# Optimization experiments

Measured on AMD Instinct MI355X. Metric: run time of the kernel, lower is better.

The kernel has to match this reference:

```python
import jax, jax.numpy as jnp
import numpy as np
from jax import lax

B, DIM, HEADS, H, W = 8, 384, 8, 64, 64
HEAD_C = DIM // HEADS        # 48 -> topk k's: 24, 32, 36, 38
HID = int(DIM * 2.66)        # 1021
EPS_LN = 1e-5
EPS_N = 1e-12
SMALL = 1e-6


def conv2d(x, w, b, pad, groups=1):
    out = lax.conv_general_dilated(
        x, w, (1, 1), [(pad, pad), (pad, pad)],
        feature_group_count=groups,
        dimension_numbers=('NCHW', 'OIHW', 'NCHW'))
    return out + b[None, :, None, None]


def l2n(x):
    # torch F.normalize(dim=-1): x / max(||x||_2, eps)
    n = jnp.linalg.norm(x, axis=-1, keepdims=True)
    return x / jnp.maximum(n, EPS_N)


def layer_norm_c(x, w, b):
    # WithBias LayerNorm over channel dim (module does to_3d -> LN(c) -> to_4d)
    xt = jnp.transpose(x, (0, 2, 3, 1))  # b h w c
    mu = xt.mean(-1, keepdims=True)
    var = xt.var(-1, keepdims=True)      # unbiased=False
    y = (xt - mu) / jnp.sqrt(var + EPS_LN) * w + b
    return jnp.transpose(y, (0, 3, 1, 2))


def setup_inputs() -> dict:
    key = jax.random.key(0)
    ks = iter(jax.random.split(key, 40))
    rn = lambda shape, s=0.02: jax.random.normal(next(ks), shape, jnp.float32) * s
    return dict(
        x=jax.random.normal(next(ks), (B, DIM, H, W), jnp.float32),
        spf=jax.random.normal(next(ks), (1, 3, H, W), jnp.float32),
        ln1_w=jnp.ones((DIM,)), ln1_b=jnp.zeros((DIM,)),
        qkv_w=rn((3 * DIM, DIM, 1, 1)), qkv_b=jnp.zeros((3 * DIM,)),
        qkvdw_w=rn((3 * DIM, 1, 3, 3)), qkvdw_b=jnp.zeros((3 * DIM,)),
        proj_w=rn((DIM, 3, 3, 3)), proj_b=jnp.zeros((DIM,)),
        temperature=jnp.ones((HEADS, 1, 1)),
        a1=jnp.array([0.2]), a2=jnp.array([0.2]),
        a3=jnp.array([0.2]), a4=jnp.array([0.2]),
        wmix=jnp.ones((2,)),
        pout_w=rn((DIM, DIM, 1, 1)), pout_b=jnp.zeros((DIM,)),
        ln2_w=jnp.ones((DIM,)), ln2_b=jnp.zeros((DIM,)),
        pin_w=rn((2 * HID, DIM, 1, 1)), pin_b=jnp.zeros((2 * HID,)),
        dw_w=rn((HID, 1, 3, 3)), dw_b=jnp.zeros((HID,)),
        lin_w=rn((HID, HID)), lin_b=jnp.zeros((HID,)),
        adj_w=rn((HID, 2 * HID, 1, 1)), adj_b=jnp.zeros((HID,)),
        fout_w=rn((DIM, HID, 1, 1)), fout_b=jnp.zeros((DIM,)),
    )


def reference(x, spf, ln1_w, ln1_b, qkv_w, qkv_b, qkvdw_w, qkvdw_b,
              proj_w, proj_b, temperature, a1, a2, a3, a4, wmix,
              pout_w, pout_b, ln2_w, ln2_b, pin_w, pin_b, dw_w, dw_b,
              lin_w, lin_b, adj_w, adj_b, fout_w, fout_b):
    # ---------- Attention ----------
    xn = layer_norm_c(x, ln1_w, ln1_b)
    qkv = conv2d(conv2d(xn, qkv_w, qkv_b, 0), qkvdw_w, qkvdw_b, 1, groups=3 * DIM)
    q, k, v = jnp.split(qkv, 3, axis=1)
    q1 = l2n(q)                               # normalize along W axis
    spm = conv2d(jnp.broadcast_to(l2n(spf), (B, 3, H, W)), proj_w, proj_b, 1)
    qs = l2n((q1 * spm).reshape(B, HEADS, HEAD_C, H * W))
    kr = l2n(k.reshape(B, HEADS, HEAD_C, H * W))
    vr = v.reshape(B, HEADS, HEAD_C, H * W)
    attn = jnp.einsum('bhcn,bhdn->bhcd', qs, kr) * temperature[None]

    def masked_sm(kk):
        thr = lax.top_k(attn, kk)[0][..., -1:]  # k-th largest per row
        return jax.nn.softmax(jnp.where(attn >= thr, attn, attn * SMALL), axis=-1)

    attn0 = jax.nn.relu(attn)
    wsm = jax.nn.softmax(wmix)
    topks = [HEAD_C // 2, 2 * HEAD_C // 3, 3 * HEAD_C // 4, 4 * HEAD_C // 5]
    out = jnp.zeros((B, HEADS, HEAD_C, H * W), attn.dtype)
    for kk, c in zip(topks, [a1, a2, a3, a4]):
        blend = attn0 * wsm[0] + masked_sm(kk) * wsm[1]
        out = out + c * jnp.einsum('bhcd,bhdn->bhcn', blend, vr)
    out = out.reshape(B, DIM, H, W)
    x = x + conv2d(out, pout_w, pout_b, 0)

    # ---------- FeedForward ----------
    xn2 = layer_norm_c(x, ln2_w, ln2_b)
    p = conv2d(xn2, pin_w, pin_b, 0)
    x1, x2 = jnp.split(p, 2, axis=1)
    x1d = conv2d(x1, dw_w, dw_b, 1, groups=HID)
    x2l = jnp.einsum('bchw,oc->bohw', x2, lin_w) + lin_b[None, :, None, None]
    cat = jnp.concatenate([x1d, x2l], axis=1)    # [B, 2*HID, H, W]
    y1 = conv2d(cat, adj_w, adj_b, 0)
    y2 = y1  # second cat is identical under the intended (non-buggy) reading
    f = jax.nn.gelu(y1, approximate=False) * y2
    return x + conv2d(f, fout_w, fout_b, 0)
```

## Files before the change

### kernel.cpp

```cpp
#include <hip/hip_runtime.h>
#include <math.h>

typedef long long i64;
typedef unsigned short u16;
typedef unsigned int u32;

#define DIMC 384
#define DIM3 1152
#define HC 48
#define HWN 4096

using bf16x8 = __attribute__((ext_vector_type(8))) short;
using f32x4 = __attribute__((ext_vector_type(4))) float;

__device__ __forceinline__ float bf2f(u16 u) { u32 x = ((u32)u) << 16; return __uint_as_float(x); }
__device__ __forceinline__ u16 f2bf(float f) {
  u32 u = __float_as_uint(f);
  u32 r = u + 0x7FFFu + ((u >> 16) & 1u);
  return (u16)(r >> 16);
}

__device__ __forceinline__ void gld_lds16(const u16* g, u16* l) {
  __builtin_amdgcn_global_load_lds(
      (const __attribute__((address_space(1))) void*)g,
      (__attribute__((address_space(3))) void*)l, 16, 0, 0);
}


__global__ void zero_kernel(float* __restrict__ p, int n) {
  int i = blockIdx.x * 256 + threadIdx.x;
  if (i < n) p[i] = 0.f;
}

__device__ __forceinline__ float ld_as_f(const float* p) { return *p; }
__device__ __forceinline__ float ld_as_f(const u16* p) { return bf2f(*p); }

template <typename T>
__global__ void stats_kernel(const T* __restrict__ x, float* __restrict__ mu,
                             float* __restrict__ rs, int npix4) {
  int idx = blockIdx.x * 256 + threadIdx.x;
  if (idx >= npix4) return;
  int pg = idx * 4;
  int b = pg >> 12, p = pg & 4095;
  const T* xp = x + ((i64)b * DIMC) * HWN + p;
  float s0 = 0.f, s1 = 0.f, s2 = 0.f, s3 = 0.f;
  float q0 = 0.f, q1 = 0.f, q2 = 0.f, q3 = 0.f;
  for (int c = 0; c < DIMC; ++c) {
    const T* rp = xp + (i64)c * HWN;
    float v0 = ld_as_f(rp), v1 = ld_as_f(rp + 1), v2 = ld_as_f(rp + 2), v3 = ld_as_f(rp + 3);
    s0 += v0; s1 += v1; s2 += v2; s3 += v3;
    q0 += v0 * v0; q1 += v1 * v1; q2 += v2 * v2; q3 += v3 * v3;
  }
  const float inv = 1.f / DIMC;
  float4 m = make_float4(s0 * inv, s1 * inv, s2 * inv, s3 * inv);
  float4 r;
  r.x = rsqrtf(q0 * inv - m.x * m.x + 1e-5f);
  r.y = rsqrtf(q1 * inv - m.y * m.y + 1e-5f);
  r.z = rsqrtf(q2 * inv - m.z * m.z + 1e-5f);
  r.w = rsqrtf(q3 * inv - m.w * m.w + 1e-5f);
  *(float4*)(mu + (i64)pg) = m;
  *(float4*)(rs + (i64)pg) = r;
}

template <typename T>
__global__ __launch_bounds__(256) void ln_t_kernel(
    const T* __restrict__ x, const float* __restrict__ mu, const float* __restrict__ rs,
    const float* __restrict__ g, const float* __restrict__ bb, u16* __restrict__ y) {
  __shared__ u16 tile[64][66];
  int p0 = blockIdx.x * 64, c0 = blockIdx.y * 64, b = blockIdx.z;
  int t = threadIdx.x;
  int tp = t & 63, tq = t >> 6;
  float m = mu[b * 4096 + p0 + tp], r = rs[b * 4096 + p0 + tp];
  const T* xp = x + (i64)b * DIMC * HWN + (i64)c0 * 4096 + p0;
#pragma unroll
  for (int i = 0; i < 16; ++i) {
    int c = tq + i * 4;
    float v = ld_as_f(xp + (i64)c * 4096 + tp);
    tile[c][tp] = f2bf((v - m) * r * g[c0 + c] + bb[c0 + c]);
  }
  __syncthreads();
#pragma unroll
  for (int i = 0; i < 16; ++i) {
    int p = tq + i * 4;
    y[((i64)b * 4096 + p0 + p) * 384 + c0 + tp] = tile[tp][p];
  }
}

__global__ __launch_bounds__(256) void dw8_kernel(const u16* __restrict__ in, int ldin,
                                                  const float* __restrict__ w,
                                                  const float* __restrict__ bias,
                                                  u16* __restrict__ out, int ldo, int CH) {
  int t = threadIdx.x;
  int g = t & 31;
  int s = t >> 5;
  int c0 = (blockIdx.y * 32 + g) * 4;
  if (c0 >= ldo) return;
  i64 p0 = (i64)blockIdx.x * 32 + s * 4;
  i64 pb = p0 & ~4095LL;
  int sp = (int)(p0 & 4095);
  int y = sp >> 6, x0 = sp & 63;
  float wv[9][4];
  float acc[4][4];
#pragma unroll
  for (int cc = 0; cc < 4; ++cc) {
    bool val = (c0 + cc) < CH;
    float bv = val ? bias[c0 + cc] : 0.f;
#pragma unroll
    for (int i = 0; i < 4; ++i) acc[i][cc] = bv;
#pragma unroll
    for (int j = 0; j < 9; ++j) wv[j][cc] = val ? w[(c0 + cc) * 9 + j] : 0.f;
  }
#pragma unroll
  for (int dy = 0; dy < 3; ++dy) {
    int yy = y - 1 + dy;
    if ((unsigned)yy >= 64u) continue;
    float row[6][4];
#pragma unroll
    for (int dx = 0; dx < 6; ++dx) {
      int xx = x0 - 1 + dx;
      if ((unsigned)xx < 64u) {
        ushort4 v = *(const ushort4*)(in + (pb + yy * 64 + xx) * ldin + c0);
        row[dx][0] = bf2f(v.x); row[dx][1] = bf2f(v.y);
        row[dx][2] = bf2f(v.z); row[dx][3] = bf2f(v.w);
      } else {
        row[dx][0] = 0.f; row[dx][1] = 0.f; row[dx][2] = 0.f; row[dx][3] = 0.f;
      }
    }
#pragma unroll
    for (int i = 0; i < 4; ++i)
#pragma unroll
      for (int dx = 0; dx < 3; ++dx)
#pragma unroll
        for (int cc = 0; cc < 4; ++cc)
          acc[i][cc] += row[i + dx][cc] * wv[dy * 3 + dx][cc];
  }
#pragma unroll
  for (int i = 0; i < 4; ++i) {
    ushort4 o;
    o.x = (c0 + 0 < CH) ? f2bf(acc[i][0]) : (u16)0;
    o.y = (c0 + 1 < CH) ? f2bf(acc[i][1]) : (u16)0;
    o.z = (c0 + 2 < CH) ? f2bf(acc[i][2]) : (u16)0;
    o.w = (c0 + 3 < CH) ? f2bf(acc[i][3]) : (u16)0;
    *(ushort4*)(out + (p0 + i) * ldo + c0) = o;
  }
}

__global__ __launch_bounds__(192) void dwqnorm_kernel(
    const u16* __restrict__ qkv, const float* __restrict__ w9,
    const float* __restrict__ bias, const float* __restrict__ spm,
    const u16* __restrict__ kv, u16* __restrict__ QS,
    float* __restrict__ qssq, float* __restrict__ kssq) {
  int y = blockIdx.x;
  int b = blockIdx.y;
  int c = blockIdx.z * 192 + threadIdx.x;
  float wv[9];
#pragma unroll
  for (int j = 0; j < 9; ++j) wv[j] = w9[c * 9 + j];
  float bv = bias[c];
  float acc[64];
#pragma unroll
  for (int i = 0; i < 64; ++i) acc[i] = bv;
  i64 rowbase = (i64)b * 4096;
#pragma unroll
  for (int dy = 0; dy < 3; ++dy) {
    int yy = y - 1 + dy;
    if ((unsigned)yy >= 64u) continue;
    const u16* rp = qkv + (rowbase + yy * 64) * 1152 + c;
    float w0 = wv[dy * 3 + 0], w1 = wv[dy * 3 + 1], w2 = wv[dy * 3 + 2];
#pragma unroll
    for (int xi = 0; xi < 64; ++xi) {
      float v = bf2f(rp[(i64)xi * 1152]);
      if (xi > 0) acc[xi - 1] += v * w2;
      acc[xi] += v * w1;
      if (xi < 63) acc[xi + 1] += v * w0;
    }
  }
  float qs = 0.f;
#pragma unroll
  for (int i = 0; i < 64; ++i) qs += acc[i] * acc[i];
  float rw = 1.f / fmaxf(sqrtf(qs), 1e-12f);
  float ps = 0.f;
  const float* sp = spm + (i64)(y * 64) * 384 + c;
  u16* qp = QS + (rowbase + y * 64) * 384 + c;
#pragma unroll
  for (int i = 0; i < 64; ++i) {
    float u = acc[i] * rw * sp[(i64)i * 384];
    qp[(i64)i * 384] = f2bf(u);
    ps += u * u;
  }
  atomicAdd(&qssq[b * 384 + c], ps);
  float ks = 0.f;
  const u16* kp = kv + (rowbase + y * 64) * 768 + c;
#pragma unroll
  for (int i = 0; i < 64; ++i) {
    float kvv = bf2f(kp[(i64)i * 768]);
    ks += kvv * kvv;
  }
  atomicAdd(&kssq[b * 384 + c], ks);
}

__global__ void l2row_kernel(const float* __restrict__ in, float* __restrict__ out) {
  int r = blockIdx.x;
  int lane = threadIdx.x;
  float v = in[r * 64 + lane];
  float ss = v * v;
  for (int o = 32; o > 0; o >>= 1) ss += __shfl_xor(ss, o);
  float n = fmaxf(sqrtf(ss), 1e-12f);
  out[r * 64 + lane] = v / n;
}

__global__ void spm_kernel(const float* __restrict__ s, const float* __restrict__ w,
                           const float* __restrict__ bias, float* __restrict__ out) {
  int idx = blockIdx.x * 256 + threadIdx.x;
  int c = idx % 384, p = idx / 384;
  int xc = p & 63, yr = p >> 6;
  const float* wp = w + c * 27;
  float acc = bias[c];
  for (int ic = 0; ic < 3; ++ic)
    for (int dy = -1; dy <= 1; ++dy) {
      int yy = yr + dy; if ((unsigned)yy >= 64u) continue;
      for (int dx = -1; dx <= 1; ++dx) {
        int xx = xc + dx; if ((unsigned)xx >= 64u) continue;
        acc += s[ic * 4096 + yy * 64 + xx] * wp[ic * 9 + (dy + 1) * 3 + (dx + 1)];
      }
    }
  out[idx] = acc;
}

__global__ __launch_bounds__(256) void attnS_kernel(const u16* __restrict__ QS,
                                                    const u16* __restrict__ kv,
                                                    float* __restrict__ attnP) {
  int ksp = blockIdx.x;
  int bh = blockIdx.y;
  int b = bh >> 3, h = bh & 7;
  __shared__ float qsm[64][49];
  __shared__ float ksm[64][49];
  int t = threadIdx.x, tc = t & 15, td = t >> 4;
  float acc[3][3] = {{0.f}};
  for (int sub = 0; sub < 4; ++sub) {
    i64 nb = (i64)b * 4096 + ksp * 256 + sub * 64;
    __syncthreads();
    for (int l = t; l < 4096; l += 256) {
      int row = l >> 6, cq = l & 63;
      if (cq < 48) {
        qsm[row][cq] = bf2f(QS[(nb + row) * 384 + h * 48 + cq]);
        ksm[row][cq] = bf2f(kv[(nb + row) * 768 + h * 48 + cq]);
      }
    }
    __syncthreads();
#pragma unroll 4
    for (int nn = 0; nn < 64; ++nn) {
      float a0 = qsm[nn][tc], a1 = qsm[nn][tc + 16], a2 = qsm[nn][tc + 32];
      float b0 = ksm[nn][td], b1 = ksm[nn][td + 16], b2 = ksm[nn][td + 32];
      acc[0][0] += a0 * b0; acc[0][1] += a0 * b1; acc[0][2] += a0 * b2;
      acc[1][0] += a1 * b0; acc[1][1] += a1 * b1; acc[1][2] += a1 * b2;
      acc[2][0] += a2 * b0; acc[2][1] += a2 * b1; acc[2][2] += a2 * b2;
    }
  }
  float* ap = attnP + ((i64)bh * 16 + ksp) * 2304;
#pragma unroll
  for (int i = 0; i < 3; ++i)
#pragma unroll
    for (int j = 0; j < 3; ++j)
      ap[(tc + 16 * i) * HC + (td + 16 * j)] = acc[i][j];
}

__global__ void blend_kernel(const float* __restrict__ attnP, const float* __restrict__ qssq,
                             const float* __restrict__ kssq, const float* __restrict__ temp,
                             const float* __restrict__ wmix, const float* __restrict__ pa1,
                             const float* __restrict__ pa2, const float* __restrict__ pa3,
                             const float* __restrict__ pa4, float* __restrict__ comb) {
  int row = blockIdx.x * 4 + (threadIdx.x >> 6);
  int lane = threadIdx.x & 63;
  int bh = row / 48, cc = row - bh * 48;
  int b = bh >> 3, h = bh & 7;
  float a;
  if (lane < 48) {
    const float* pp = attnP + ((i64)bh * 16) * 2304 + cc * 48 + lane;
    float s = 0.f;
#pragma unroll
    for (int sp = 0; sp < 16; ++sp) s += pp[(i64)sp * 2304];
    float qn = 1.f / fmaxf(sqrtf(qssq[b * 384 + h * 48 + cc]), 1e-12f);
    float kn = 1.f / fmaxf(sqrtf(kssq[b * 384 + h * 48 + lane]), 1e-12f);
    a = s * qn * kn * temp[h];
  } else {
    a = -INFINITY;
  }
  int rank = 0;
  for (int j = 0; j < 48; ++j) {
    float aj = __shfl(a, j);
    rank += (aj > a) ? 1 : 0;
  }
  float w0 = wmix[0], w1 = wmix[1];
  float wm = fmaxf(w0, w1);
  float e0 = expf(w0 - wm), e1 = expf(w1 - wm);
  float ws0 = e0 / (e0 + e1), ws1 = e1 / (e0 + e1);
  float c1 = pa1[0], c2 = pa2[0], c3 = pa3[0], c4 = pa4[0];
  float outv = ws0 * (c1 + c2 + c3 + c4) * fmaxf(a, 0.f);
  const int kks[4] = {24, 32, 36, 38};
  const float cs[4] = {c1, c2, c3, c4};
#pragma unroll
  for (int q = 0; q < 4; ++q) {
    float mv = (lane < 48) ? ((rank < kks[q]) ? a : a * 1e-6f) : -INFINITY;
    float mx = mv;
    for (int o = 32; o > 0; o >>= 1) mx = fmaxf(mx, __shfl_xor(mx, o));
    float e = (lane < 48) ? expf(mv - mx) : 0.f;
    float s = e;
    for (int o = 32; o > 0; o >>= 1) s += __shfl_xor(s, o);
    outv += ws1 * cs[q] * (e / s);
  }
  if (lane < 48) comb[(i64)row * 48 + lane] = outv;
}

__global__ __launch_bounds__(384) void combv_kernel(const u16* __restrict__ kv,
                                                    const float* __restrict__ comb,
                                                    u16* __restrict__ AO) {
  __shared__ float Vs[4][8][49];
  i64 p0 = (i64)blockIdx.x * 4;
  int b = (int)(p0 >> 12);
  int t = threadIdx.x;
  int h = t / 48, cc = t - h * 48;
#pragma unroll
  for (int px = 0; px < 4; ++px)
    Vs[px][h][cc] = bf2f(kv[(p0 + px) * 768 + 384 + t]);
  __syncthreads();
  float cr[48];
  const float* cp = comb + ((i64)(b * 8 + h) * 48 + cc) * 48;
#pragma unroll
  for (int d = 0; d < 48; d += 4) {
    float4 v = *(const float4*)(cp + d);
    cr[d] = v.x; cr[d + 1] = v.y; cr[d + 2] = v.z; cr[d + 3] = v.w;
  }
#pragma unroll
  for (int px = 0; px < 4; ++px) {
    float s = 0.f;
#pragma unroll
    for (int d = 0; d < 48; ++d) s += cr[d] * Vs[px][h][d];
    AO[(p0 + px) * 384 + t] = f2bf(s);
  }
}

__global__ void matvec_kernel(const float* __restrict__ Wm, int ldw, int koff,
                              const float* __restrict__ v, const float* __restrict__ add,
                              float* __restrict__ out, int K) {
  int ro = blockIdx.x;
  int t = threadIdx.x;
  const float* wp = Wm + (i64)ro * ldw + koff;
  float s = 0.f;
  for (int k = t; k < K; k += 256) s += wp[k] * v[k];
  __shared__ float sred[256];
  sred[t] = s;
  __syncthreads();
  for (int o = 128; o > 0; o >>= 1) {
    if (t < o) sred[t] += sred[t + o];
    __syncthreads();
  }
  if (t == 0) out[ro] = sred[0] + (add ? add[ro] : 0.f);
}

__global__ __launch_bounds__(256) void gemm64_kernel(
    const float* __restrict__ W, int ldw,
    const float* __restrict__ X,
    float* __restrict__ Y,
    int M, int N, int K, int ksplit) {
  int nt = blockIdx.x, mt = blockIdx.y;
  int ks = blockIdx.z;
  int kchunk = (((K + ksplit - 1) / ksplit) + 15) & ~15;
  int kbeg = ks * kchunk;
  int kend = min(K, kbeg + kchunk);
  __shared__ float As[16][68];
  __shared__ float Bs[16][68];
  int t = threadIdx.x, tx = t & 15, ty = t >> 4;
  int m0 = mt * 64, n0 = nt * 64;
  float acc[4][4];
#pragma unroll
  for (int i = 0; i < 4; ++i)
#pragma unroll
    for (int j = 0; j < 4; ++j) acc[i][j] = 0.f;
  for (int k0 = kbeg; k0 < kend; k0 += 16) {
    int kk = t & 15;
#pragma unroll
    for (int r = 0; r < 4; ++r) {
      int mm = (t >> 4) + r * 16;
      int gm = m0 + mm, gk = k0 + kk;
      As[kk][mm] = (gm < M && gk < kend) ? W[(i64)gm * ldw + gk] : 0.f;
    }
    int nn = t & 63;
#pragma unroll
    for (int r = 0; r < 4; ++r) {
      int k2 = (t >> 6) + r * 4;
      int gk = k0 + k2;
      Bs[k2][nn] = (gk < kend && n0 + nn < N) ? X[(i64)gk * N + n0 + nn] : 0.f;
    }
    __syncthreads();
#pragma unroll
    for (int kk3 = 0; kk3 < 16; ++kk3) {
      float4 av = *(const float4*)&As[kk3][ty * 4];
      float4 bv = *(const float4*)&Bs[kk3][tx * 4];
      float aa[4] = {av.x, av.y, av.z, av.w};
      float bb2[4] = {bv.x, bv.y, bv.z, bv.w};
#pragma unroll
      for (int i = 0; i < 4; ++i)
#pragma unroll
        for (int j = 0; j < 4; ++j) acc[i][j] += aa[i] * bb2[j];
    }
    __syncthreads();
  }
#pragma unroll
  for (int i = 0; i < 4; ++i) {
    int gm = m0 + ty * 4 + i;
    if (gm >= M || n0 + tx * 4 >= N) continue;
    for (int j = 0; j < 4; ++j) atomicAdd(&Y[(i64)gm * N + n0 + tx * 4 + j], acc[i][j]);
  }
}

__global__ void pack_w_kernel(const float* __restrict__ W, int ldw, int koff, int M, int K,
                              int KS, u16* __restrict__ out, int nfrag) {
  int tid = blockIdx.x * 256 + threadIdx.x;
  int lane = tid & 63;
  int idx = tid >> 6;
  if (idx >= nfrag * KS) return;
  int ks = idx % KS, fm = idx / KS;
  int row = fm * 16 + (lane & 15);
  int kb = ks * 32 + (lane >> 4) * 8;
  union { u16 us[8]; uint4 q; } u;
#pragma unroll
  for (int j = 0; j < 8; ++j) {
    int k = kb + j;
    u.us[j] = (row < M && k < K) ? f2bf(W[(i64)row * ldw + koff + k]) : (u16)0;
  }
  *(uint4*)(out + (i64)idx * 512 + lane * 8) = u.q;
}

template <int NF>
__global__ __launch_bounds__(NF * 32) void gemm_nk_kernel(
    const u16* __restrict__ A1, int lda1, int KS1, const u16* __restrict__ Wp1,
    const u16* __restrict__ A2, int lda2, int KS2, const u16* __restrict__ Wp2,
    int nfrag, const float* __restrict__ bias,
    const void* __restrict__ Res, float* __restrict__ Yf, u16* __restrict__ Yh,
    int ldo, int M, int epi) {
  __shared__ __align__(16) u16 Ls[2][NF + 8][512];
  int t = threadIdx.x, lane = t & 63, w = t >> 6;
  int wn = w >> 1, wm = w & 1;
  i64 n0 = (i64)blockIdx.x * (NF * 16);
  int mt = blockIdx.y;

  f32x4 acc[4][4];
#pragma unroll
  for (int i = 0; i < 4; ++i)
#pragma unroll
    for (int r = 0; r < 4; ++r) acc[i][r] = (f32x4){0.f, 0.f, 0.f, 0.f};

  auto stage = [&](int kt, int buf) {
    const u16* A; int lda; const u16* Wp; int KSc; int ks;
    if (kt < KS1) { A = A1; lda = lda1; Wp = Wp1; KSc = KS1; ks = kt; }
    else { A = A2; lda = lda2; Wp = Wp2; KSc = KS2; ks = kt - KS1; }
#pragma unroll
    for (int j = 0; j < 2; ++j) {
      int f = w * 2 + j;
      const u16* srcA = A + (n0 + f * 16 + (lane & 15)) * (i64)lda + ks * 32 + (lane >> 4) * 8;
      gld_lds16(srcA, &Ls[buf][f][0]);
    }
    if constexpr (NF == 8) {
#pragma unroll
      for (int j = 0; j < 2; ++j) {
        int f = w * 2 + j;
        int fmc = min(mt * 8 + f, nfrag - 1);
        gld_lds16(Wp + ((i64)fmc * KSc + ks) * 512 + lane * 8, &Ls[buf][NF + f][0]);
      }
    } else {
      int fmc = min(mt * 8 + w, nfrag - 1);
      gld_lds16(Wp + ((i64)fmc * KSc + ks) * 512 + lane * 8, &Ls[buf][NF + w][0]);
    }
  };

  int KT = KS1 + KS2;
  stage(0, 0);
  __syncthreads();
  int s = 0;
  for (int kt = 0; kt < KT; ++kt) {
    if (kt + 1 < KT) stage(kt + 1, s ^ 1);
    bf16x8 af[4], wf[4];
#pragma unroll
    for (int i = 0; i < 4; ++i) {
      af[i] = *reinterpret_cast<const bf16x8*>(&Ls[s][wn * 4 + i][lane * 8]);
      wf[i] = *reinterpret_cast<const bf16x8*>(&Ls[s][NF + wm * 4 + i][lane * 8]);
    }
#pragma unroll
    for (int i = 0; i < 4; ++i)
#pragma unroll
      for (int r = 0; r < 4; ++r)
        acc[i][r] = __builtin_amdgcn_mfma_f32_16x16x32_bf16(af[i], wf[r], acc[i][r], 0, 0, 0);
    __syncthreads();
    s ^= 1;
  }

#pragma unroll
  for (int i = 0; i < 4; ++i) {
    int nbase = (int)n0 + (wn * 4 + i) * 16 + ((lane >> 4) << 2);
#pragma unroll
    for (int r = 0; r < 4; ++r) {
      int m = mt * 128 + (wm * 4 + r) * 16 + (lane & 15);
      if (epi == 1 || epi == 3) {
        if (m < M) {
          float bv = bias[m];
          int b = nbase >> 12, p = nbase & 4095;
          i64 off = ((i64)b * DIMC + m) * 4096 + p;
          if (epi == 1) {
            float4 rv = *(const float4*)((const float*)Res + off);
            ushort4 o;
            o.x = f2bf(acc[i][r][0] + bv + rv.x);
            o.y = f2bf(acc[i][r][1] + bv + rv.y);
            o.z = f2bf(acc[i][r][2] + bv + rv.z);
            o.w = f2bf(acc[i][r][3] + bv + rv.w);
            *(ushort4*)(Yh + off) = o;
          } else {
            ushort4 rv = *(const ushort4*)((const u16*)Res + off);
            float4 o;
            o.x = acc[i][r][0] + bv + bf2f(rv.x);
            o.y = acc[i][r][1] + bv + bf2f(rv.y);
            o.z = acc[i][r][2] + bv + bf2f(rv.z);
            o.w = acc[i][r][3] + bv + bf2f(rv.w);
            *(float4*)(Yf + off) = o;
          }
        }
      } else {
        if (m < ldo) {
          float bv = (m < M) ? bias[m] : 0.f;
#pragma unroll
          for (int ii = 0; ii < 4; ++ii) {
            float v = acc[i][r][ii] + bv;
            if (epi == 2) {
              float gg = 0.5f * v * (1.f + erff(v * 0.70710678118f));
              v = gg * v;
            }
            if (m >= M) v = 0.f;
            Yh[(i64)(nbase + ii) * ldo + m] = f2bf(v);
          }
        }
      }
    }
  }
}


extern "C" void kernel_launch(void* const* d_in, const int* in_sizes, int n_in,
                              void* d_out, int out_size, void* d_ws, size_t ws_size,
                              hipStream_t stream) {
  (void)in_sizes; (void)n_in; (void)out_size;
  const float* x       = (const float*)d_in[0];
  const float* spf     = (const float*)d_in[1];
  const float* ln1_w   = (const float*)d_in[2];
  const float* ln1_b   = (const float*)d_in[3];
  const float* qkv_w   = (const float*)d_in[4];
  const float* qkv_b   = (const float*)d_in[5];
  const float* qkvdw_w = (const float*)d_in[6];
  const float* qkvdw_b = (const float*)d_in[7];
  const float* proj_w  = (const float*)d_in[8];
  const float* proj_b  = (const float*)d_in[9];
  const float* temp    = (const float*)d_in[10];
  const float* a1      = (const float*)d_in[11];
  const float* a2      = (const float*)d_in[12];
  const float* a3      = (const float*)d_in[13];
  const float* a4      = (const float*)d_in[14];
  const float* wmix    = (const float*)d_in[15];
  const float* pout_w  = (const float*)d_in[16];
  const float* pout_b  = (const float*)d_in[17];
  const float* ln2_w   = (const float*)d_in[18];
  const float* ln2_b   = (const float*)d_in[19];
  const float* pin_w   = (const float*)d_in[20];
  const float* pin_b   = (const float*)d_in[21];
  const float* dw_w    = (const float*)d_in[22];
  const float* dw_b    = (const float*)d_in[23];
  const float* lin_w   = (const float*)d_in[24];
  const float* lin_b   = (const float*)d_in[25];
  const float* adj_w   = (const float*)d_in[26];
  const float* adj_b   = (const float*)d_in[27];
  const float* fout_w  = (const float*)d_in[28];
  const float* fout_b  = (const float*)d_in[29];
  float* out = (float*)d_out;
  float* ws = (float*)d_ws;

  const i64 PLANE = (i64)DIMC * HWN;
  const i64 FIXED = 5326592;
  const i64 PER = 8439808;
  int C = 8;
  while (C > 1 && (size_t)(FIXED + PER * C) * 4 > ws_size) C >>= 1;
  if ((size_t)(FIXED + PER * C) * 4 > ws_size) return;
  int nch = 8 / C;

  float* SPM   = ws;
  float* W2v   = SPM + 1572864;
  float* W3v   = W2v + 392064;
  float* b2v   = W3v + 392064;
  float* b3v   = b2v + 1024;
  float* spfn  = b3v + 1024;
  float* mu1   = spfn + 12288;
  float* rs1   = mu1 + 32768;
  float* mu2   = rs1 + 32768;
  float* rs2   = mu2 + 32768;
  float* qssq  = rs2 + 32768;
  float* kssq  = qssq + 3072;
  float* packbase = kssq + 3072;
  u16* qkv_wp  = (u16*)packbase;
  u16* pout_wp = qkv_wp + 884736;
  u16* pin_wp  = pout_wp + 294912;
  u16* adj1_wp = pin_wp + 786432;
  u16* W3_wp   = adj1_wp + 2097152;
  u16* fout_wp = W3_wp + 786432;
  float* dyn   = packbase + 2818048;
  float* attnP = dyn;
  float* comb  = attnP + (i64)C * 294912;
  float* R1    = comb + (i64)C * 18432;
  float* R2    = R1 + (i64)C * 2359296;
  float* R3    = R2 + (i64)C * 2097152;
  float* R4    = R3 + (i64)C * 2097152;
  float* R5    = R4 + (i64)C * 786432;

  zero_kernel<<<dim3(3063), dim3(256), 0, stream>>>(W2v, 784128);
  matvec_kernel<<<dim3(1021), dim3(256), 0, stream>>>(lin_w, 1021, 0, pin_b + 1021, lin_b, b2v, 1021);
  gemm64_kernel<<<dim3(6, 16, 8), dim3(256), 0, stream>>>(
      lin_w, 1021, pin_w + (i64)1021 * 384, W2v, 1021, 384, 1021, 8);
  matvec_kernel<<<dim3(1021), dim3(256), 0, stream>>>(adj_w, 2042, 1021, b2v, adj_b, b3v, 1021);
  gemm64_kernel<<<dim3(6, 16, 8), dim3(256), 0, stream>>>(
      adj_w + 1021, 2042, W2v, W3v, 1021, 384, 1021, 8);

  pack_w_kernel<<<dim3(216), dim3(256), 0, stream>>>(qkv_w, 384, 0, 1152, 384, 12, qkv_wp, 72);
  pack_w_kernel<<<dim3(72), dim3(256), 0, stream>>>(pout_w, 384, 0, 384, 384, 12, pout_wp, 24);
  pack_w_kernel<<<dim3(192), dim3(256), 0, stream>>>(pin_w, 384, 0, 1021, 384, 12, pin_wp, 64);
  pack_w_kernel<<<dim3(512), dim3(256), 0, stream>>>(adj_w, 2042, 0, 1021, 1021, 32, adj1_wp, 64);
  pack_w_kernel<<<dim3(192), dim3(256), 0, stream>>>(W3v, 384, 0, 1021, 384, 12, W3_wp, 64);
  pack_w_kernel<<<dim3(192), dim3(256), 0, stream>>>(fout_w, 1021, 0, 384, 1021, 32, fout_wp, 24);

  l2row_kernel<<<dim3(192), dim3(64), 0, stream>>>(spf, spfn);
  spm_kernel<<<dim3(6144), dim3(256), 0, stream>>>(spfn, proj_w, proj_b, SPM);
  stats_kernel<float><<<dim3(32), dim3(256), 0, stream>>>(x, mu1, rs1, 8192);

  for (int ch = 0; ch < nch; ++ch) {
    int b0 = ch * C;
    const float* xb = x + (i64)b0 * PLANE;
    float* outb = out + (i64)b0 * PLANE;
    const float* m1 = mu1 + (i64)b0 * HWN;
    const float* r1 = rs1 + (i64)b0 * HWN;

    u16* Xbf    = (u16*)R3;
    u16* qkv_bf = (u16*)R1;
    u16* kvb    = (u16*)R2;
    u16* QS     = (u16*)R3;
    u16* AO     = (u16*)R3;
    u16* xatt   = (u16*)R4;
    u16* xn2    = (u16*)R5;
    u16* x1     = (u16*)R1;
    u16* x1d    = (u16*)R2;
    u16* fbf    = (u16*)R3;

    int NB16 = C * 16;
    int NB8  = C * 32;

    zero_kernel<<<dim3((2 * C * 384 + 255) / 256), dim3(256), 0, stream>>>(qssq, 2 * C * 384);
    ln_t_kernel<float><<<dim3(64, 6, C), dim3(256), 0, stream>>>(xb, m1, r1, ln1_w, ln1_b, Xbf);
    gemm_nk_kernel<16><<<dim3(NB16, 9), dim3(512), 0, stream>>>(
        Xbf, 384, 12, qkv_wp, nullptr, 0, 0, nullptr, 72,
        qkv_b, nullptr, nullptr, qkv_bf, 1152, 1152, 0);
    dw8_kernel<<<dim3(C * 128, 6), dim3(256), 0, stream>>>(
        qkv_bf + 384, 1152, qkvdw_w + 384 * 9, qkvdw_b + 384, kvb, 768, 768);
    dwqnorm_kernel<<<dim3(64, C, 2), dim3(192), 0, stream>>>(
        qkv_bf, qkvdw_w, qkvdw_b, SPM, kvb, QS, qssq, kssq);
    attnS_kernel<<<dim3(16, C * 8), dim3(256), 0, stream>>>(QS, kvb, attnP);
    blend_kernel<<<dim3(96 * C), dim3(256), 0, stream>>>(attnP, qssq, kssq, temp, wmix,
                                                         a1, a2, a3, a4, comb);
    combv_kernel<<<dim3(C * 1024), dim3(384), 0, stream>>>(kvb, comb, AO);
    gemm_nk_kernel<8><<<dim3(NB8, 3), dim3(256), 0, stream>>>(
        AO, 384, 12, pout_wp, nullptr, 0, 0, nullptr, 24,
        pout_b, xb, nullptr, xatt, 0, 384, 1);

    stats_kernel<u16><<<dim3((C * 1024 + 255) / 256), dim3(256), 0, stream>>>(xatt, mu2, rs2,
                                                                              C * 1024);
    ln_t_kernel<u16><<<dim3(64, 6, C), dim3(256), 0, stream>>>(xatt, mu2, rs2, ln2_w, ln2_b, xn2);
    gemm_nk_kernel<16><<<dim3(NB16, 8), dim3(512), 0, stream>>>(
        xn2, 384, 12, pin_wp, nullptr, 0, 0, nullptr, 64,
        pin_b, nullptr, nullptr, x1, 1024, 1021, 0);
    dw8_kernel<<<dim3(C * 128, 8), dim3(256), 0, stream>>>(
        x1, 1024, dw_w, dw_b, x1d, 1024, 1021);
    gemm_nk_kernel<16><<<dim3(NB16, 8), dim3(512), 0, stream>>>(
        x1d, 1024, 32, adj1_wp, xn2, 384, 12, W3_wp, 64,
        b3v, nullptr, nullptr, fbf, 1024, 1021, 2);
    gemm_nk_kernel<8><<<dim3(NB8, 3), dim3(256), 0, stream>>>(
        fbf, 1024, 32, fout_wp, nullptr, 0, 0, nullptr, 24,
        fout_b, xatt, outb, nullptr, 0, 384, 3);
  }
}
```

Measured before the change: 1.092 ms.

## Compute folded FFN weight products with bf16 MFMA GEMM and shrink workspace

The weight-folding products lin_w·pin_w2 and adj_w2·W2 were computed by a scalar fp32 split-K GEMM with atomics. They now run on the existing bf16 MFMA gemm_nk kernel, after conversion and transposed packing kernels prepare the operands. The per-chunk buffer layout is also reorganised so regions are reused more tightly, which lowers the workspace footprint and may allow larger batch chunks. The trade-off is that the folded weights are rounded to bf16 at an intermediate stage, and a few extra small launches are added.

```diff
diff --git a/kernel.cpp b/kernel.cpp
--- a/kernel.cpp
+++ b/kernel.cpp
@@ -19,6 +19,10 @@
   u32 r = u + 0x7FFFu + ((u >> 16) & 1u);
   return (u16)(r >> 16);
 }
+__device__ __forceinline__ u16 to_bf16(float f) { return f2bf(f); }
+__device__ __forceinline__ u16 to_bf16(u16 u) { return u; }
+__device__ __forceinline__ float ld_as_f(const float* p) { return *p; }
+__device__ __forceinline__ float ld_as_f(const u16* p) { return bf2f(*p); }
 
 __device__ __forceinline__ void gld_lds16(const u16* g, u16* l) {
   __builtin_amdgcn_global_load_lds(
@@ -32,8 +36,12 @@
   if (i < n) p[i] = 0.f;
 }
 
-__device__ __forceinline__ float ld_as_f(const float* p) { return *p; }
-__device__ __forceinline__ float ld_as_f(const u16* p) { return bf2f(*p); }
+__global__ void cvt_pad_kernel(const float* __restrict__ src, int lds, int M, int K,
+                               u16* __restrict__ out) {
+  int idx = blockIdx.x * 256 + threadIdx.x;
+  int r = idx >> 10, k = idx & 1023;
+  out[idx] = (r < M && k < K) ? f2bf(src[(i64)r * lds + k]) : (u16)0;
+}
 
 template <typename T>
 __global__ void stats_kernel(const T* __restrict__ x, float* __restrict__ mu,
@@ -358,63 +366,8 @@
   if (t == 0) out[ro] = sred[0] + (add ? add[ro] : 0.f);
 }
 
-__global__ __launch_bounds__(256) void gemm64_kernel(
-    const float* __restrict__ W, int ldw,
-    const float* __restrict__ X,
-    float* __restrict__ Y,
-    int M, int N, int K, int ksplit) {
-  int nt = blockIdx.x, mt = blockIdx.y;
-  int ks = blockIdx.z;
-  int kchunk = (((K + ksplit - 1) / ksplit) + 15) & ~15;
-  int kbeg = ks * kchunk;
-  int kend = min(K, kbeg + kchunk);
-  __shared__ float As[16][68];
-  __shared__ float Bs[16][68];
-  int t = threadIdx.x, tx = t & 15, ty = t >> 4;
-  int m0 = mt * 64, n0 = nt * 64;
-  float acc[4][4];
-#pragma unroll
-  for (int i = 0; i < 4; ++i)
-#pragma unroll
-    for (int j = 0; j < 4; ++j) acc[i][j] = 0.f;
-  for (int k0 = kbeg; k0 < kend; k0 += 16) {
-    int kk = t & 15;
-#pragma unroll
-    for (int r = 0; r < 4; ++r) {
-      int mm = (t >> 4) + r * 16;
-      int gm = m0 + mm, gk = k0 + kk;
-      As[kk][mm] = (gm < M && gk < kend) ? W[(i64)gm * ldw + gk] : 0.f;
-    }
-    int nn = t & 63;
-#pragma unroll
-    for (int r = 0; r < 4; ++r) {
-      int k2 = (t >> 6) + r * 4;
-      int gk = k0 + k2;
-      Bs[k2][nn] = (gk < kend && n0 + nn < N) ? X[(i64)gk * N + n0 + nn] : 0.f;
-    }
-    __syncthreads();
-#pragma unroll
-    for (int kk3 = 0; kk3 < 16; ++kk3) {
-      float4 av = *(const float4*)&As[kk3][ty * 4];
-      float4 bv = *(const float4*)&Bs[kk3][tx * 4];
-      float aa[4] = {av.x, av.y, av.z, av.w};
-      float bb2[4] = {bv.x, bv.y, bv.z, bv.w};
-#pragma unroll
-      for (int i = 0; i < 4; ++i)
-#pragma unroll
-        for (int j = 0; j < 4; ++j) acc[i][j] += aa[i] * bb2[j];
-    }
-    __syncthreads();
-  }
-#pragma unroll
-  for (int i = 0; i < 4; ++i) {
-    int gm = m0 + ty * 4 + i;
-    if (gm >= M || n0 + tx * 4 >= N) continue;
-    for (int j = 0; j < 4; ++j) atomicAdd(&Y[(i64)gm * N + n0 + tx * 4 + j], acc[i][j]);
-  }
-}
-
-__global__ void pack_w_kernel(const float* __restrict__ W, int ldw, int koff, int M, int K,
+template <typename T>
+__global__ void pack_w_kernel(const T* __restrict__ W, int ldw, int koff, int M, int K,
                               int KS, u16* __restrict__ out, int nfrag) {
   int tid = blockIdx.x * 256 + threadIdx.x;
   int lane = tid & 63;
@@ -427,7 +380,26 @@
 #pragma unroll
   for (int j = 0; j < 8; ++j) {
     int k = kb + j;
-    u.us[j] = (row < M && k < K) ? f2bf(W[(i64)row * ldw + koff + k]) : (u16)0;
+    u.us[j] = (row < M && k < K) ? to_bf16(W[(i64)row * ldw + koff + k]) : (u16)0;
+  }
+  *(uint4*)(out + (i64)idx * 512 + lane * 8) = u.q;
+}
+
+template <typename T>
+__global__ void pack_wT_kernel(const T* __restrict__ src, int ldk, i64 kbase, int M, int K,
+                               int KS, u16* __restrict__ out, int nfrag) {
+  int tid = blockIdx.x * 256 + threadIdx.x;
+  int lane = tid & 63;
+  int idx = tid >> 6;
+  if (idx >= nfrag * KS) return;
+  int ks = idx % KS, fm = idx / KS;
+  int row = fm * 16 + (lane & 15);
+  int kb = ks * 32 + (lane >> 4) * 8;
+  union { u16 us[8]; uint4 q; } u;
+#pragma unroll
+  for (int j = 0; j < 8; ++j) {
+    int k = kb + j;
+    u.us[j] = (row < M && k < K) ? to_bf16(src[(kbase + k) * (i64)ldk + row]) : (u16)0;
   }
   *(uint4*)(out + (i64)idx * 512 + lane * 8) = u.q;
 }
@@ -582,19 +554,18 @@
   float* ws = (float*)d_ws;
 
   const i64 PLANE = (i64)DIMC * HWN;
-  const i64 FIXED = 5326592;
-  const i64 PER = 8439808;
+  const i64 FIXED = 4543488;
+  const i64 PER = 6342656;
   int C = 8;
   while (C > 1 && (size_t)(FIXED + PER * C) * 4 > ws_size) C >>= 1;
   if ((size_t)(FIXED + PER * C) * 4 > ws_size) return;
   int nch = 8 / C;
 
   float* SPM   = ws;
-  float* W2v   = SPM + 1572864;
-  float* W3v   = W2v + 392064;
-  float* b2v   = W3v + 392064;
+  float* b2v   = SPM + 1572864;
   float* b3v   = b2v + 1024;
-  float* spfn  = b3v + 1024;
+  float* zbias = b3v + 1024;
+  float* spfn  = zbias + 1024;
   float* mu1   = spfn + 12288;
   float* rs1   = mu1 + 32768;
   float* mu2   = rs1 + 32768;
@@ -609,28 +580,43 @@
   u16* W3_wp   = adj1_wp + 2097152;
   u16* fout_wp = W3_wp + 786432;
   float* dyn   = packbase + 2818048;
+
   float* attnP = dyn;
   float* comb  = attnP + (i64)C * 294912;
-  float* R1    = comb + (i64)C * 18432;
-  float* R2    = R1 + (i64)C * 2359296;
-  float* R3    = R2 + (i64)C * 2097152;
-  float* R4    = R3 + (i64)C * 2097152;
-  float* R5    = R4 + (i64)C * 786432;
-
-  zero_kernel<<<dim3(3063), dim3(256), 0, stream>>>(W2v, 784128);
+  float* RA    = comb + (i64)C * 18432;
+  float* RD    = RA + (i64)C * 786432;
+  float* RB    = RD + (i64)C * 786432;
+  float* RC    = RB + (i64)C * 2359296;
+
+  u16* linbf    = (u16*)dyn;
+  u16* adjbf    = linbf + 1048576;
+  u16* W2bf     = adjbf + 1048576;
+  u16* W3bf     = W2bf + 393216;
+  u16* pin2T_wp = W3bf + 393216;
+  u16* W2T_wp   = pin2T_wp + 393216;
+
+  zero_kernel<<<dim3(4), dim3(256), 0, stream>>>(zbias, 1024);
   matvec_kernel<<<dim3(1021), dim3(256), 0, stream>>>(lin_w, 1021, 0, pin_b + 1021, lin_b, b2v, 1021);
-  gemm64_kernel<<<dim3(6, 16, 8), dim3(256), 0, stream>>>(
-      lin_w, 1021, pin_w + (i64)1021 * 384, W2v, 1021, 384, 1021, 8);
   matvec_kernel<<<dim3(1021), dim3(256), 0, stream>>>(adj_w, 2042, 1021, b2v, adj_b, b3v, 1021);
-  gemm64_kernel<<<dim3(6, 16, 8), dim3(256), 0, stream>>>(
-      adj_w + 1021, 2042, W2v, W3v, 1021, 384, 1021, 8);
-
-  pack_w_kernel<<<dim3(216), dim3(256), 0, stream>>>(qkv_w, 384, 0, 1152, 384, 12, qkv_wp, 72);
-  pack_w_kernel<<<dim3(72), dim3(256), 0, stream>>>(pout_w, 384, 0, 384, 384, 12, pout_wp, 24);
-  pack_w_kernel<<<dim3(192), dim3(256), 0, stream>>>(pin_w, 384, 0, 1021, 384, 12, pin_wp, 64);
-  pack_w_kernel<<<dim3(512), dim3(256), 0, stream>>>(adj_w, 2042, 0, 1021, 1021, 32, adj1_wp, 64);
-  pack_w_kernel<<<dim3(192), dim3(256), 0, stream>>>(W3v, 384, 0, 1021, 384, 12, W3_wp, 64);
-  pack_w_kernel<<<dim3(192), dim3(256), 0, stream>>>(fout_w, 1021, 0, 384, 1021, 32, fout_wp, 24);
+  cvt_pad_kernel<<<dim3(4096), dim3(256), 0, stream>>>(lin_w, 1021, 1021, 1021, linbf);
+  cvt_pad_kernel<<<dim3(4096), dim3(256), 0, stream>>>(adj_w + 1021, 2042, 1021, 1021, adjbf);
+  pack_wT_kernel<float><<<dim3(192), dim3(256), 0, stream>>>(pin_w, 384, 1021, 384, 1021, 32,
+                                                             pin2T_wp, 24);
+  gemm_nk_kernel<8><<<dim3(8, 3), dim3(256), 0, stream>>>(
+      linbf, 1024, 32, pin2T_wp, nullptr, 0, 0, nullptr, 24,
+      zbias, nullptr, nullptr, W2bf, 384, 384, 0);
+  pack_wT_kernel<u16><<<dim3(192), dim3(256), 0, stream>>>(W2bf, 384, 0, 384, 1021, 32,
+                                                           W2T_wp, 24);
+  gemm_nk_kernel<8><<<dim3(8, 3), dim3(256), 0, stream>>>(
+      adjbf, 1024, 32, W2T_wp, nullptr, 0, 0, nullptr, 24,
+      zbias, nullptr, nullptr, W3bf, 384, 384, 0);
+  pack_w_kernel<u16><<<dim3(192), dim3(256), 0, stream>>>(W3bf, 384, 0, 1021, 384, 12, W3_wp, 64);
+
+  pack_w_kernel<float><<<dim3(216), dim3(256), 0, stream>>>(qkv_w, 384, 0, 1152, 384, 12, qkv_wp, 72);
+  pack_w_kernel<float><<<dim3(72), dim3(256), 0, stream>>>(pout_w, 384, 0, 384, 384, 12, pout_wp, 24);
+  pack_w_kernel<float><<<dim3(192), dim3(256), 0, stream>>>(pin_w, 384, 0, 1021, 384, 12, pin_wp, 64);
+  pack_w_kernel<float><<<dim3(512), dim3(256), 0, stream>>>(adj_w, 2042, 0, 1021, 1021, 32, adj1_wp, 64);
+  pack_w_kernel<float><<<dim3(192), dim3(256), 0, stream>>>(fout_w, 1021, 0, 384, 1021, 32, fout_wp, 24);
 
   l2row_kernel<<<dim3(192), dim3(64), 0, stream>>>(spf, spfn);
   spm_kernel<<<dim3(6144), dim3(256), 0, stream>>>(spfn, proj_w, proj_b, SPM);
@@ -643,16 +629,16 @@
     const float* m1 = mu1 + (i64)b0 * HWN;
     const float* r1 = rs1 + (i64)b0 * HWN;
 
-    u16* Xbf    = (u16*)R3;
-    u16* qkv_bf = (u16*)R1;
-    u16* kvb    = (u16*)R2;
-    u16* QS     = (u16*)R3;
-    u16* AO     = (u16*)R3;
-    u16* xatt   = (u16*)R4;
-    u16* xn2    = (u16*)R5;
-    u16* x1     = (u16*)R1;
-    u16* x1d    = (u16*)R2;
-    u16* fbf    = (u16*)R3;
+    u16* Xbf    = (u16*)RA;
+    u16* qkv_bf = (u16*)RB;
+    u16* kvb    = (u16*)RC;
+    u16* QS     = (u16*)RA;
+    u16* AO     = (u16*)RA;
+    u16* xatt   = (u16*)RD;
+    u16* xn2    = (u16*)RA;
+    u16* x1     = (u16*)RB;
+    u16* x1d    = (u16*)RC;
+    u16* fbf    = (u16*)RB;
 
     int NB16 = C * 16;
     int NB8  = C * 32;
```

After: 928.4 us. 1.18x faster.
